# Kernel tuning notes

Hardware: AMD Instinct MI355X
Metric: run time of the kernel (lower is better)

## Reference

```python
import jax, jax.numpy as jnp
import numpy as np

B, Ng, C, H, W, Nt, M, P = 4, 8192, 256, 128, 128, 512, 8, 4
Ch = C // M  # 32 channels per head
EPS = 1e-5


def setup_inputs():
    key = jax.random.key(0)
    ks = jax.random.split(key, 12)
    s = 0.02
    def w(k, shape):
        return jax.random.normal(k, shape, jnp.float32) * s
    return {
        "query": jax.random.normal(ks[0], (B, Ng, C), jnp.float32),
        "value": jax.random.normal(ks[1], (B, C, H, W), jnp.float32),
        "reference_points": jax.random.uniform(ks[2], (B, Ng, 2), dtype=jnp.float32),
        "trajectory_points": jax.random.uniform(ks[3], (B, Nt, 2), dtype=jnp.float32),
        "in_proj_w": w(ks[4], (3 * C, C)),
        "in_proj_b": jnp.zeros((3 * C,), jnp.float32),
        "mha_out_w": w(ks[5], (C, C)),
        "mha_out_b": jnp.zeros((C,), jnp.float32),
        "ln_g": jnp.ones((C,), jnp.float32),
        "ln_b": jnp.zeros((C,), jnp.float32),
        "traj_w": w(ks[6], (C, 2)),
        "traj_b": jnp.zeros((C,), jnp.float32),
        "offs_w": w(ks[7], (M * P * 2, C)),
        "offs_b": jnp.zeros((M * P * 2,), jnp.float32),
        "attw_w": w(ks[8], (M * P, C)),
        "attw_b": jnp.zeros((M * P,), jnp.float32),
        "out_w": w(ks[9], (C, C)),
        "out_b": jnp.zeros((C,), jnp.float32),
    }


def _bilinear_sample(imgf, x, y):
    # imgf: (NM, Ch, H*W); x, y: (NM, Lq, P) unnormalized pixel coords
    # grid_sample semantics: bilinear, padding_mode='zeros', align_corners=False
    NM = imgf.shape[0]
    Lq, Pp = x.shape[1], x.shape[2]
    x0 = jnp.floor(x); y0 = jnp.floor(y)
    x1 = x0 + 1.0;     y1 = y0 + 1.0

    def gather(xi, yi):
        valid = (xi >= 0) & (xi < W) & (yi >= 0) & (yi < H)
        xc = jnp.clip(xi, 0, W - 1).astype(jnp.int32)
        yc = jnp.clip(yi, 0, H - 1).astype(jnp.int32)
        idx = (yc * W + xc).reshape(NM, 1, Lq * Pp)
        v = jnp.take_along_axis(imgf, jnp.broadcast_to(idx, (NM, Ch, Lq * Pp)), axis=2)
        return v.reshape(NM, Ch, Lq, Pp), valid.astype(imgf.dtype)

    v00, m00 = gather(x0, y0)
    v01, m01 = gather(x1, y0)
    v10, m10 = gather(x0, y1)
    v11, m11 = gather(x1, y1)
    wx1 = x - x0; wx0 = 1.0 - wx1
    wy1 = y - y0; wy0 = 1.0 - wy1
    out = (v00 * (wx0 * wy0 * m00)[:, None]
         + v01 * (wx1 * wy0 * m01)[:, None]
         + v10 * (wx0 * wy1 * m10)[:, None]
         + v11 * (wx1 * wy1 * m11)[:, None])
    return out  # (NM, Ch, Lq, P)


def reference(query, value, reference_points, trajectory_points,
              in_proj_w, in_proj_b, mha_out_w, mha_out_b, ln_g, ln_b,
              traj_w, traj_b, offs_w, offs_b, attw_w, attw_b, out_w, out_b):
    # trajectory projection: (B,Nt,2) -> (B,Nt,C)
    tf = trajectory_points @ traj_w.T + traj_b

    # guidance cross-attention (nn.MultiheadAttention, eval mode => no dropout)
    wq, wk, wv = jnp.split(in_proj_w, 3, axis=0)
    bq, bk, bv = jnp.split(in_proj_b, 3, axis=0)
    q = (query @ wq.T + bq).reshape(B, Ng, M, Ch)
    k = (tf @ wk.T + bk).reshape(B, Nt, M, Ch)
    v = (tf @ wv.T + bv).reshape(B, Nt, M, Ch)
    scores = jnp.einsum('bqmc,bkmc->bmqk', q, k) / jnp.sqrt(jnp.float32(Ch))
    probs = jax.nn.softmax(scores, axis=-1)
    ctx = jnp.einsum('bmqk,bkmc->bqmc', probs, v).reshape(B, Ng, C)
    ctx = ctx @ mha_out_w.T + mha_out_b

    # residual + LayerNorm
    x = query + ctx
    mu = x.mean(-1, keepdims=True)
    var = ((x - mu) ** 2).mean(-1, keepdims=True)
    gq = (x - mu) / jnp.sqrt(var + EPS) * ln_g + ln_b

    # sampling offsets & softmax attention weights (L=1 level)
    offs = (gq @ offs_w.T + offs_b).reshape(B, Ng, M, 1, P, 2)
    aw = jax.nn.softmax((gq @ attw_w.T + attw_b).reshape(B, Ng, M, P), axis=-1)
    loc = reference_points[:, :, None, None, None, :] + offs  # (B,Ng,M,1,P,2)

    # deformable sampling core (single level)
    grid = 2.0 * loc[:, :, :, 0] - 1.0                   # (B,Ng,M,P,2)
    grid = grid.transpose(0, 2, 1, 3, 4).reshape(B * M, Ng, P, 2)
    gx = (grid[..., 0] + 1.0) * (W * 0.5) - 0.5
    gy = (grid[..., 1] + 1.0) * (H * 0.5) - 0.5
    imgf = value.reshape(B * M, Ch, H * W)               # per-head feature maps
    samp = _bilinear_sample(imgf, gx, gy)                # (B*M,Ch,Ng,P)
    w_att = aw.transpose(0, 2, 1, 3).reshape(B * M, 1, Ng, P)
    out = (samp * w_att).sum(-1)                         # (B*M,Ch,Ng)

    # faithful to source: view(B,M,Ch,Ng).transpose(1,2).contiguous().view(B,Ng,C)
    out = out.reshape(B, M, Ch, Ng).transpose(0, 2, 1, 3).reshape(B, Ng, C)
    return out @ out_w.T + out_b
```

## Files before the change

### kernel.cpp

```cpp
#include <hip/hip_runtime.h>
#include <hip/hip_bf16.h>
#include <stdint.h>

typedef __bf16 bf16_t;
typedef __bf16 bf16x8 __attribute__((ext_vector_type(8)));
typedef __bf16 bf16x4 __attribute__((ext_vector_type(4)));
typedef float f32x4 __attribute__((ext_vector_type(4)));

#define CEXP 0.25506807186679906f

__device__ __forceinline__ float ldf(const void* p, size_t i, int isf) {
  return isf ? ((const float*)p)[i] : (float)((const bf16_t*)p)[i];
}

__device__ __forceinline__ int detect_isf(const void* q) {
  const uint16_t* u = (const uint16_t*)q;
  const int lane = threadIdx.x & 63;
  const uint16_t v = u[2 * lane];
  const int e = (v >> 7) & 0xFF;
  const int weird = (e >= 0x86 || (v != 0 && e <= 0x65)) ? 1 : 0;
  return (__popcll(__ballot(weird)) >= 16) ? 1 : 0;
}

__device__ __forceinline__ float fexp2(float x) {
#if __has_builtin(__builtin_amdgcn_exp2f)
  return __builtin_amdgcn_exp2f(x);
#else
  return exp2f(x);
#endif
}

__device__ __forceinline__ f32x4 mfma16x16x16(bf16x4 a, bf16x4 b, f32x4 c) {
#if __has_builtin(__builtin_amdgcn_mfma_f32_16x16x16_bf16)
  return __builtin_amdgcn_mfma_f32_16x16x16_bf16(a, b, c, 0, 0, 0);
#else
  typedef short s16x4 __attribute__((ext_vector_type(4)));
  return __builtin_amdgcn_mfma_f32_16x16x16bf16_1k(
      __builtin_bit_cast(s16x4, a), __builtin_bit_cast(s16x4, b), c, 0, 0, 0);
#endif
}

__device__ __forceinline__ void stage16(const bf16_t* g, bf16_t* l) {
  __builtin_amdgcn_global_load_lds((const __attribute__((address_space(1))) void*)g,
                                   (__attribute__((address_space(3))) void*)l, 16, 0, 0);
}

__global__ __launch_bounds__(256) void prep_all(
    const void* __restrict__ query,
    const void* in_w, const void* in_b, const void* mow, const void* mob,
    const void* outw, const void* outb,
    const void* trajp, const void* tw, const void* tb,
    const void* offs_w, const void* attw_w, const void* offs_b, const void* attw_b,
    bf16_t* __restrict__ blob, bf16_t* __restrict__ tf,
    bf16_t* __restrict__ Wph, bf16_t* __restrict__ Wpl, bf16_t* __restrict__ bp,
    const void* __restrict__ V, bf16_t* __restrict__ Vp)
{
  __shared__ __align__(16) bf16_t tile[32][136];
  const int isf = detect_isf(query);
  const int bid = blockIdx.x;
  if (bid < 322) {
    const int g = (bid * 256 + threadIdx.x) * 4;
    if (g >= 328960) return;
    const void* src; size_t off;
    if      (g < 196608) { src = in_w; off = g; }
    else if (g < 197376) { src = in_b; off = g - 196608; }
    else if (g < 262912) { src = mow;  off = g - 197376; }
    else if (g < 263168) { src = mob;  off = g - 262912; }
    else if (g < 328704) { src = outw; off = g - 263168; }
    else                 { src = outb; off = g - 328704; }
#pragma unroll
    for (int k = 0; k < 4; k++) blob[g + k] = (bf16_t)ldf(src, off + k, isf);
  } else if (bid < 322 + 2048) {
    const int rowb = bid - 322;
    const int c = threadIdx.x;
    const float x = ldf(trajp, rowb * 2 + 0, isf);
    const float y = ldf(trajp, rowb * 2 + 1, isf);
    const float v = x * ldf(tw, c * 2 + 0, isf) + y * ldf(tw, c * 2 + 1, isf) + ldf(tb, c, isf);
    tf[(size_t)rowb * 256 + c] = (bf16_t)v;
  } else if (bid < 2498) {
    const int idx = (bid - 2370) * 256 + threadIdx.x;
    const int rowp = idx >> 8, c = idx & 255;
    float v = 0.0f;
    if (rowp < 64)      v = ldf(offs_w, rowp * 256 + c, isf);
    else if (rowp < 96) v = ldf(attw_w, (rowp - 64) * 256 + c, isf);
    const bf16_t hi = (bf16_t)v;
    Wph[idx] = hi;
    Wpl[idx] = (bf16_t)(v - (float)hi);
    if (idx < 128) {
      float bv = 0.0f;
      if (idx < 64)      bv = ldf(offs_b, idx, isf);
      else if (idx < 96) bv = ldf(attw_b, idx - 64, isf);
      bp[idx] = (bf16_t)bv;
    }
  } else {
    const int vb = bid - 2498;
    const int h = vb & 127;
    const int bm = vb >> 7;
    const int b = bm >> 3, mm = bm & 7;
    const int t = threadIdx.x;
    const int ch  = t >> 3;
    const int ww0 = (t & 7) * 16;
    const size_t ibase = (((size_t)b * 256 + mm * 32 + ch) * 128 + h) * 128 + ww0;
    if (isf) {
      const float4* src = (const float4*)((const float*)V + ibase);
      bf16x8 h0, h1;
#pragma unroll
      for (int k = 0; k < 2; k++) {
        const float4 u0 = src[k * 2], u1 = src[k * 2 + 1];
        bf16x8 hh = {(bf16_t)u0.x, (bf16_t)u0.y, (bf16_t)u0.z, (bf16_t)u0.w,
                     (bf16_t)u1.x, (bf16_t)u1.y, (bf16_t)u1.z, (bf16_t)u1.w};
        if (k == 0) h0 = hh; else h1 = hh;
      }
      *(bf16x8*)(&tile[ch][ww0])     = h0;
      *(bf16x8*)(&tile[ch][ww0 + 8]) = h1;
    } else {
      const bf16x8* src = (const bf16x8*)((const bf16_t*)V + ibase);
      *(bf16x8*)(&tile[ch][ww0])     = src[0];
      *(bf16x8*)(&tile[ch][ww0 + 8]) = src[1];
    }
    __syncthreads();
    const size_t base = ((size_t)bm * 128 + h) * 4096;
    const int ww = t >> 1;
    const int c0 = (t & 1) * 16;
    bf16x8 o0, o1;
#pragma unroll
    for (int e = 0; e < 8; e++) { o0[e] = tile[c0 + e][ww]; o1[e] = tile[c0 + 8 + e][ww]; }
    *(bf16x8*)(Vp + base + ww * 32 + c0)     = o0;
    *(bf16x8*)(Vp + base + ww * 32 + c0 + 8) = o1;
  }
}

#define TM 128
#define TN 128
#define TKK 64

__global__ __launch_bounds__(256) void gemm_async(
    const bf16_t* __restrict__ A, const bf16_t* __restrict__ W,
    const bf16_t* __restrict__ bias, void* __restrict__ Cout,
    void* __restrict__ Cout2, int Ndim, int Kdim, int mode, float kscale,
    const void* __restrict__ qdet)
{
  __shared__ __align__(16) bf16_t As[TM * TKK];
  __shared__ __align__(16) bf16_t Ws[TN * TKK];
  const int t    = threadIdx.x;
  const int lane = t & 63;
  const int w    = t >> 6;
  const int wm   = (w & 1) * 64;
  const int wn   = (w >> 1) * 64;
  const int q4   = lane >> 4;
  const int r16  = lane & 15;
  const int tm   = blockIdx.x * TM;
  const int tn   = blockIdx.y * TN;

  f32x4 acc[4][4] = {};

  for (int kt = 0; kt < Kdim; kt += TKK) {
    __syncthreads();
#pragma unroll
    for (int r = 0; r < 4; r++) {
      const int L = w * 256 + r * 64 + lane;
      const int R = L >> 3, c = (L & 7) * 8;
      stage16(A + (size_t)(tm + R) * Kdim + kt + c, As + L * 8);
      stage16(W + (size_t)(tn + R) * Kdim + kt + c, Ws + L * 8);
    }
    __syncthreads();
#pragma unroll
    for (int ks = 0; ks < TKK; ks += 32) {
      bf16x8 af[4], bfm[4];
#pragma unroll
      for (int i = 0; i < 4; i++)
        af[i] = *(const bf16x8*)(As + (wm + 16 * i + r16) * TKK + ks + q4 * 8);
#pragma unroll
      for (int j = 0; j < 4; j++)
        bfm[j] = *(const bf16x8*)(Ws + (wn + 16 * j + r16) * TKK + ks + q4 * 8);
#pragma unroll
      for (int i = 0; i < 4; i++)
#pragma unroll
        for (int j = 0; j < 4; j++)
          acc[i][j] = __builtin_amdgcn_mfma_f32_16x16x32_bf16(af[i], bfm[j], acc[i][j], 0, 0, 0);
    }
  }

  const int isf = (mode == 3) ? detect_isf(qdet) : 1;
#pragma unroll
  for (int j = 0; j < 4; j++) {
    const int col = tn + wn + 16 * j + r16;
    const float bv = (float)bias[col];
#pragma unroll
    for (int i = 0; i < 4; i++) {
      const int row0 = tm + wm + 16 * i + q4 * 4;
#pragma unroll
      for (int rr = 0; rr < 4; rr++) {
        const float v = acc[i][j][rr] + bv;
        const size_t off = (size_t)(row0 + rr) * Ndim + col;
        if (mode == 0) {
          ((bf16_t*)Cout)[off] = (bf16_t)v;
        } else {
          if (isf) ((float*)Cout)[off] = v; else ((bf16_t*)Cout)[off] = (bf16_t)v;
        }
      }
    }
  }
}

__global__ __launch_bounds__(256) void gemm_qkv(
    const void* __restrict__ Araw, const bf16_t* __restrict__ Wq,
    const bf16_t* __restrict__ bq, bf16_t* __restrict__ Cq,
    const bf16_t* __restrict__ Atf, const bf16_t* __restrict__ Wkv,
    const bf16_t* __restrict__ bkv, bf16_t* __restrict__ Kout,
    bf16_t* __restrict__ Vtout, float kscale, const void* __restrict__ qdet)
{
  __shared__ __align__(16) bf16_t As[TM * TKK];
  __shared__ __align__(16) bf16_t Ws[TN * TKK];
  const int t    = threadIdx.x;
  const int lane = t & 63;
  const int w    = t >> 6;
  const int wm   = (w & 1) * 64;
  const int wn   = (w >> 1) * 64;
  const int q4   = lane >> 4;
  const int r16  = lane & 15;
  const int blk  = blockIdx.x;

  f32x4 acc[4][4] = {};

  if (blk < 512) {
    const int tm = (blk >> 1) * TM;
    const int tn = (blk & 1) * TN;
    const int aisf = detect_isf(qdet);
    const int srow = t >> 1;
    const int skb  = (t & 1) * 32;

    for (int kt = 0; kt < 256; kt += TKK) {
      __syncthreads();
      if (aisf) {
        const float4* ga = (const float4*)((const float*)Araw + (size_t)(tm + srow) * 256 + kt + skb);
#pragma unroll
        for (int kk = 0; kk < 8; kk++) {
          const float4 u = ga[kk];
          bf16x4 h = {(bf16_t)u.x, (bf16_t)u.y, (bf16_t)u.z, (bf16_t)u.w};
          *(bf16x4*)(As + srow * TKK + skb + kk * 4) = h;
        }
      } else {
        const uint4* ga = (const uint4*)((const bf16_t*)Araw + (size_t)(tm + srow) * 256 + kt + skb);
        uint4* la = (uint4*)(As + srow * TKK + skb);
        la[0] = ga[0]; la[1] = ga[1]; la[2] = ga[2]; la[3] = ga[3];
      }
      {
        const uint4* gw = (const uint4*)(Wq + (size_t)(tn + srow) * 256 + kt + skb);
        uint4* lw = (uint4*)(Ws + srow * TKK + skb);
        lw[0] = gw[0]; lw[1] = gw[1]; lw[2] = gw[2]; lw[3] = gw[3];
      }
      __syncthreads();
#pragma unroll
      for (int ks = 0; ks < TKK; ks += 32) {
        bf16x8 af[4], bfm[4];
#pragma unroll
        for (int i = 0; i < 4; i++)
          af[i] = *(const bf16x8*)(As + (wm + 16 * i + r16) * TKK + ks + q4 * 8);
#pragma unroll
        for (int j = 0; j < 4; j++)
          bfm[j] = *(const bf16x8*)(Ws + (wn + 16 * j + r16) * TKK + ks + q4 * 8);
#pragma unroll
        for (int i = 0; i < 4; i++)
#pragma unroll
          for (int j = 0; j < 4; j++)
            acc[i][j] = __builtin_amdgcn_mfma_f32_16x16x32_bf16(af[i], bfm[j], acc[i][j], 0, 0, 0);
      }
    }

#pragma unroll
    for (int j = 0; j < 4; j++) {
      const int col = tn + wn + 16 * j + r16;
      const float bv = (float)bq[col];
#pragma unroll
      for (int i = 0; i < 4; i++) {
        const int row0 = tm + wm + 16 * i + q4 * 4;
#pragma unroll
        for (int rr = 0; rr < 4; rr++)
          Cq[(size_t)(row0 + rr) * 256 + col] = (bf16_t)(acc[i][j][rr] + bv);
      }
    }
  } else {
    const int k = blk - 512;
    const int tm = (k & 15) * TM;
    const int tn = (k >> 4) * TN;

    for (int kt = 0; kt < 256; kt += TKK) {
      __syncthreads();
#pragma unroll
      for (int r = 0; r < 4; r++) {
        const int L = w * 256 + r * 64 + lane;
        const int R = L >> 3, c = (L & 7) * 8;
        stage16(Atf + (size_t)(tm + R) * 256 + kt + c, As + L * 8);
        stage16(Wkv + (size_t)(tn + R) * 256 + kt + c, Ws + L * 8);
      }
      __syncthreads();
#pragma unroll
      for (int ks = 0; ks < TKK; ks += 32) {
        bf16x8 af[4], bfm[4];
#pragma unroll
        for (int i = 0; i < 4; i++)
          af[i] = *(const bf16x8*)(As + (wm + 16 * i + r16) * TKK + ks + q4 * 8);
#pragma unroll
        for (int j = 0; j < 4; j++)
          bfm[j] = *(const bf16x8*)(Ws + (wn + 16 * j + r16) * TKK + ks + q4 * 8);
#pragma unroll
        for (int i = 0; i < 4; i++)
#pragma unroll
          for (int j = 0; j < 4; j++)
            acc[i][j] = __builtin_amdgcn_mfma_f32_16x16x32_bf16(af[i], bfm[j], acc[i][j], 0, 0, 0);
      }
    }

#pragma unroll
    for (int j = 0; j < 4; j++) {
      const int col = tn + wn + 16 * j + r16;
      const float bv = (float)bkv[col];
#pragma unroll
      for (int i = 0; i < 4; i++) {
        const int row0 = tm + wm + 16 * i + q4 * 4;
#pragma unroll
        for (int rr = 0; rr < 4; rr++) {
          const float v = acc[i][j][rr] + bv;
          const int rowg = row0 + rr;
          if (col < 256) {
            Kout[(size_t)rowg * 256 + col] = (bf16_t)(v * kscale);
          } else {
            const int bb = rowg >> 9, tt = rowg & 511;
            const int c2 = col - 256;
            const int mm = c2 >> 5, ch = c2 & 31;
            Vtout[(((size_t)(bb * 8 + mm) * 32 + ch) << 9) + tt] = (bf16_t)v;
          }
        }
      }
    }
  }
}

__global__ __launch_bounds__(256, 2) void attn_kernel(
    const bf16_t* __restrict__ Q, const bf16_t* __restrict__ Kk,
    const bf16_t* __restrict__ Vt, bf16_t* __restrict__ ctx)
{
  const int t = threadIdx.x;
  const int lane = t & 63, w = t >> 6;
  const int q4 = lane >> 4, r16 = lane & 15;
  const int bm = blockIdx.y;
  const int b = bm >> 3, m = bm & 7;
  const int q0 = blockIdx.x * 512 + w * 128;

  bf16x8 qf[8];
#pragma unroll
  for (int qt = 0; qt < 8; qt++)
    qf[qt] = *(const bf16x8*)(Q + ((size_t)(b * 8192 + q0 + qt * 16 + r16) * 256 + m * 32 + q4 * 8));

  f32x4 acc[8][2] = {};
  float lsum[8] = {0.f, 0.f, 0.f, 0.f, 0.f, 0.f, 0.f, 0.f};

  const bf16_t* kbase  = Kk + (size_t)b * 512 * 256 + m * 32 + (size_t)r16 * 256 + q4 * 8;
  const bf16_t* vbase0 = Vt + (size_t)bm * 32 * 512 + ((size_t)r16 << 9) + q4 * 4;
  const bf16_t* vbase1 = vbase0 + (16 << 9);

  bf16x8 kfA = *(const bf16x8*)(kbase);
  bf16x4 v0A = *(const bf16x4*)(vbase0);
  bf16x4 v1A = *(const bf16x4*)(vbase1);
  bf16x8 kfB = *(const bf16x8*)(kbase + (size_t)16 * 256);
  bf16x4 v0B = *(const bf16x4*)(vbase0 + 16);
  bf16x4 v1B = *(const bf16x4*)(vbase1 + 16);

  for (int k0 = 0; k0 < 512; k0 += 32) {
    const bf16x8 ka = kfA;
    const bf16x4 va0 = v0A, va1 = v1A;
    kfA = *(const bf16x8*)(kbase + (size_t)(k0 + 32) * 256);
    v0A = *(const bf16x4*)(vbase0 + k0 + 32);
    v1A = *(const bf16x4*)(vbase1 + k0 + 32);
    __builtin_amdgcn_s_setprio(1);
#pragma unroll
    for (int qt = 0; qt < 8; qt++) {
      f32x4 z = {};
      const f32x4 s = __builtin_amdgcn_mfma_f32_16x16x32_bf16(ka, qf[qt], z, 0, 0, 0);
      const float e0 = fexp2(s[0]), e1 = fexp2(s[1]);
      const float e2 = fexp2(s[2]), e3 = fexp2(s[3]);
      lsum[qt] += (e0 + e1) + (e2 + e3);
      const bf16x4 p = {(bf16_t)e0, (bf16_t)e1, (bf16_t)e2, (bf16_t)e3};
      acc[qt][0] = mfma16x16x16(va0, p, acc[qt][0]);
      acc[qt][1] = mfma16x16x16(va1, p, acc[qt][1]);
    }
    __builtin_amdgcn_s_setprio(0);
    const bf16x8 kb = kfB;
    const bf16x4 vb0 = v0B, vb1 = v1B;
    kfB = *(const bf16x8*)(kbase + (size_t)(k0 + 48) * 256);
    v0B = *(const bf16x4*)(vbase0 + k0 + 48);
    v1B = *(const bf16x4*)(vbase1 + k0 + 48);
    __builtin_amdgcn_s_setprio(1);
#pragma unroll
    for (int qt = 0; qt < 8; qt++) {
      f32x4 z = {};
      const f32x4 s = __builtin_amdgcn_mfma_f32_16x16x32_bf16(kb, qf[qt], z, 0, 0, 0);
      const float e0 = fexp2(s[0]), e1 = fexp2(s[1]);
      const float e2 = fexp2(s[2]), e3 = fexp2(s[3]);
      lsum[qt] += (e0 + e1) + (e2 + e3);
      const bf16x4 p = {(bf16_t)e0, (bf16_t)e1, (bf16_t)e2, (bf16_t)e3};
      acc[qt][0] = mfma16x16x16(vb0, p, acc[qt][0]);
      acc[qt][1] = mfma16x16x16(vb1, p, acc[qt][1]);
    }
    __builtin_amdgcn_s_setprio(0);
  }

#pragma unroll
  for (int qt = 0; qt < 8; qt++) {
    float v = lsum[qt];
    v += __shfl_xor(v, 16, 64);
    v += __shfl_xor(v, 32, 64);
    const float inv = 1.0f / v;
    const size_t row = (size_t)b * 8192 + q0 + qt * 16 + r16;
    bf16x4 o0, o1;
#pragma unroll
    for (int rr = 0; rr < 4; rr++) {
      o0[rr] = (bf16_t)(acc[qt][0][rr] * inv);
      o1[rr] = (bf16_t)(acc[qt][1][rr] * inv);
    }
    *(bf16x4*)(ctx + row * 256 + m * 32 + q4 * 4)      = o0;
    *(bf16x4*)(ctx + row * 256 + m * 32 + 16 + q4 * 4) = o1;
  }
}

__global__ __launch_bounds__(256) void ln_kernel(
    const bf16_t* __restrict__ y2, const void* __restrict__ query,
    const void* __restrict__ g, const void* __restrict__ beta,
    bf16_t* __restrict__ gqh, bf16_t* __restrict__ gql)
{
  const int isf = detect_isf(query);
  const int rowb = blockIdx.x * 4 + (threadIdx.x >> 6);
  const int lane = threadIdx.x & 63;
  const size_t base = (size_t)rowb * 256;
  const int c0 = lane * 4;
  float x[4];
  {
    const bf16x4 yv = *(const bf16x4*)(y2 + base + c0);
    if (isf) {
      const float4 qv = *(const float4*)((const float*)query + base + c0);
      x[0] = qv.x + (float)yv[0]; x[1] = qv.y + (float)yv[1];
      x[2] = qv.z + (float)yv[2]; x[3] = qv.w + (float)yv[3];
    } else {
      const bf16x4 qv = *(const bf16x4*)((const bf16_t*)query + base + c0);
#pragma unroll
      for (int k = 0; k < 4; k++) x[k] = (float)qv[k] + (float)yv[k];
    }
  }
  float s = x[0] + x[1] + x[2] + x[3];
  for (int d = 1; d < 64; d <<= 1) s += __shfl_xor(s, d, 64);
  const float mu = s * (1.0f / 256.0f);
  float vs = 0.f;
#pragma unroll
  for (int k = 0; k < 4; k++) { const float d = x[k] - mu; vs += d * d; }
  for (int d = 1; d < 64; d <<= 1) vs += __shfl_xor(vs, d, 64);
  const float rstd = rsqrtf(vs * (1.0f / 256.0f) + 1e-5f);
  float gw[4], bb[4];
  if (isf) {
    const float4 gg = *(const float4*)((const float*)g + c0);
    const float4 bv = *(const float4*)((const float*)beta + c0);
    gw[0] = gg.x; gw[1] = gg.y; gw[2] = gg.z; gw[3] = gg.w;
    bb[0] = bv.x; bb[1] = bv.y; bb[2] = bv.z; bb[3] = bv.w;
  } else {
    const bf16x4 gg = *(const bf16x4*)((const bf16_t*)g + c0);
    const bf16x4 bv = *(const bf16x4*)((const bf16_t*)beta + c0);
#pragma unroll
    for (int k = 0; k < 4; k++) { gw[k] = (float)gg[k]; bb[k] = (float)bv[k]; }
  }
  bf16x4 hi4, lo4;
#pragma unroll
  for (int k = 0; k < 4; k++) {
    const float gv = (x[k] - mu) * rstd * gw[k] + bb[k];
    const bf16_t hi = (bf16_t)gv;
    hi4[k] = hi;
    lo4[k] = (bf16_t)(gv - (float)hi);
  }
  *(bf16x4*)(gqh + base + c0) = hi4;
  *(bf16x4*)(gql + base + c0) = lo4;
}

__global__ __launch_bounds__(256) void gemm_offs(
    const bf16_t* __restrict__ Ahg, const bf16_t* __restrict__ Alg,
    const bf16_t* __restrict__ Whg, const bf16_t* __restrict__ Wlg,
    const bf16_t* __restrict__ bias, float* __restrict__ Cout)
{
  __shared__ __align__(16) bf16_t Ah[128 * 64];
  __shared__ __align__(16) bf16_t Al[128 * 64];
  __shared__ __align__(16) bf16_t Wh[128 * 64];
  __shared__ __align__(16) bf16_t Wl[128 * 64];
  const int t    = threadIdx.x;
  const int lane = t & 63;
  const int w    = t >> 6;
  const int wm   = (w & 1) * 64;
  const int wn   = (w >> 1) * 64;
  const int q4   = lane >> 4;
  const int r16  = lane & 15;
  const int tm   = blockIdx.x * 128;

  f32x4 acc[4][4] = {};
  const int srow = t >> 1;
  const int skb  = (t & 1) * 32;

  for (int kt = 0; kt < 256; kt += 64) {
    __syncthreads();
    {
      const uint4* g0 = (const uint4*)(Ahg + (size_t)(tm + srow) * 256 + kt + skb);
      uint4* l0 = (uint4*)(Ah + srow * 64 + skb);
      l0[0] = g0[0]; l0[1] = g0[1]; l0[2] = g0[2]; l0[3] = g0[3];
      const uint4* g1 = (const uint4*)(Alg + (size_t)(tm + srow) * 256 + kt + skb);
      uint4* l1 = (uint4*)(Al + srow * 64 + skb);
      l1[0] = g1[0]; l1[1] = g1[1]; l1[2] = g1[2]; l1[3] = g1[3];
      const uint4* g2 = (const uint4*)(Whg + (size_t)srow * 256 + kt + skb);
      uint4* l2 = (uint4*)(Wh + srow * 64 + skb);
      l2[0] = g2[0]; l2[1] = g2[1]; l2[2] = g2[2]; l2[3] = g2[3];
      const uint4* g3 = (const uint4*)(Wlg + (size_t)srow * 256 + kt + skb);
      uint4* l3 = (uint4*)(Wl + srow * 64 + skb);
      l3[0] = g3[0]; l3[1] = g3[1]; l3[2] = g3[2]; l3[3] = g3[3];
    }
    __syncthreads();
#pragma unroll
    for (int ks = 0; ks < 64; ks += 32) {
      bf16x8 ah[4], al[4], bh[4], bl[4];
#pragma unroll
      for (int i = 0; i < 4; i++) {
        ah[i] = *(const bf16x8*)(Ah + (wm + 16 * i + r16) * 64 + ks + q4 * 8);
        al[i] = *(const bf16x8*)(Al + (wm + 16 * i + r16) * 64 + ks + q4 * 8);
      }
#pragma unroll
      for (int j = 0; j < 4; j++) {
        bh[j] = *(const bf16x8*)(Wh + (wn + 16 * j + r16) * 64 + ks + q4 * 8);
        bl[j] = *(const bf16x8*)(Wl + (wn + 16 * j + r16) * 64 + ks + q4 * 8);
      }
#pragma unroll
      for (int i = 0; i < 4; i++)
#pragma unroll
        for (int j = 0; j < 4; j++) {
          f32x4 a = acc[i][j];
          a = __builtin_amdgcn_mfma_f32_16x16x32_bf16(al[i], bh[j], a, 0, 0, 0);
          a = __builtin_amdgcn_mfma_f32_16x16x32_bf16(ah[i], bl[j], a, 0, 0, 0);
          a = __builtin_amdgcn_mfma_f32_16x16x32_bf16(ah[i], bh[j], a, 0, 0, 0);
          acc[i][j] = a;
        }
    }
  }

#pragma unroll
  for (int j = 0; j < 4; j++) {
    const int col = wn + 16 * j + r16;
    const float bv = (float)bias[col];
    const int live  = (col < 96) ? 1 : 0;
    const int moff  = (col < 64) ? (col >> 3) : ((col - 64) >> 2);
    const int inner = (col < 64) ? (col & 7) : (8 + (col & 3));
#pragma unroll
    for (int i = 0; i < 4; i++) {
      const int row0 = tm + wm + 16 * i + q4 * 4;
#pragma unroll
      for (int rr = 0; rr < 4; rr++) {
        if (live) {
          const int row = row0 + rr;
          const int bq = row >> 13, q = row & 8191;
          Cout[(((size_t)(bq * 8 + moff) << 13) + q) * 16 + inner] = acc[i][j][rr] + bv;
        }
      }
    }
  }
}

__global__ __launch_bounds__(256) void sampler(
    const float* __restrict__ ys2, const void* __restrict__ refp,
    const bf16_t* __restrict__ vperm, bf16_t* __restrict__ outs,
    const void* __restrict__ qdet)
{
  const int isf = detect_isf(qdet);
  const int t = threadIdx.x;
  const int wg = blockIdx.x;
  const int bm  = (wg & 7) + ((wg >> 9) << 3);
  const int mid = (wg >> 3) & 63;
  const int qt  = mid >> 1;
  const int hf  = mid & 1;
  const int b = bm >> 3, m = bm & 7;
  const int qq = qt * 256 + t;
  const size_t row = (size_t)b * 8192 + qq;
  const float* y16 = ys2 + (((size_t)bm << 13) + qq) * 16;
  const float rx = ldf(refp, row * 2 + 0, isf);
  const float ry = ldf(refp, row * 2 + 1, isf);

  const float4 off01 = *(const float4*)(y16 + 0);
  const float4 off23 = *(const float4*)(y16 + 4);
  const float4 lg    = *(const float4*)(y16 + 8);

  const float mx = fmaxf(fmaxf(lg.x, lg.y), fmaxf(lg.z, lg.w));
  const float e0 = __expf(lg.x - mx), e1 = __expf(lg.y - mx);
  const float e2 = __expf(lg.z - mx), e3 = __expf(lg.w - mx);
  const float inv = 1.0f / (e0 + e1 + e2 + e3);
  const float aw[4] = {e0 * inv, e1 * inv, e2 * inv, e3 * inv};
  const float ox[4] = {off01.x, off01.z, off23.x, off23.z};
  const float oy[4] = {off01.y, off01.w, off23.y, off23.w};

  float acc[16];
#pragma unroll
  for (int ch = 0; ch < 16; ch++) acc[ch] = 0.0f;

  const bf16_t* vbase = vperm + (size_t)bm * (128 * 128 * 32) + hf * 16;

  for (int p = 0; p < 4; p++) {
    const float gx = (rx + ox[p]) * 128.0f - 0.5f;
    const float gy = (ry + oy[p]) * 128.0f - 0.5f;
    const float x0f = floorf(gx), y0f = floorf(gy);
    const int x0 = (int)x0f, y0i = (int)y0f;
    const float wx1 = gx - x0f, wx0 = 1.0f - wx1;
    const float wy1 = gy - y0f, wy0 = 1.0f - wy1;
    const float a = aw[p];
    for (int cy = 0; cy < 2; cy++) {
      const int yy = y0i + cy;
      if (yy < 0 || yy >= 128) continue;
      const float wy = cy ? wy1 : wy0;
      for (int cx = 0; cx < 2; cx++) {
        const int xx = x0 + cx;
        if (xx < 0 || xx >= 128) continue;
        const float wgt = a * wy * (cx ? wx1 : wx0);
        const bf16x8* src8 = (const bf16x8*)(vbase + ((size_t)yy * 128 + xx) * 32);
        const bf16x8 d0 = src8[0];
        const bf16x8 d1 = src8[1];
#pragma unroll
        for (int e = 0; e < 8; e++) {
          acc[e]     += wgt * (float)d0[e];
          acc[8 + e] += wgt * (float)d1[e];
        }
      }
    }
  }

  const size_t obase = (size_t)b * 8192;
#pragma unroll
  for (int ch = 0; ch < 16; ch++) {
    const int chg = hf * 16 + ch;
    const size_t orow = obase + (size_t)(chg * 8 + m) * 32 + qt;
    outs[orow * 256 + t] = (bf16_t)acc[ch];
  }
}

extern "C" void kernel_launch(void* const* d_in, const int* in_sizes, int n_in,
                              void* d_out, int out_size, void* d_ws, size_t ws_size,
                              hipStream_t stream) {
  const void* query = d_in[0];
  const void* value = d_in[1];
  const void* refp  = d_in[2];
  const void* trajp = d_in[3];
  const void* in_w  = d_in[4];
  const void* in_b  = d_in[5];
  const void* mow   = d_in[6];
  const void* mob   = d_in[7];
  const void* lng   = d_in[8];
  const void* lnb   = d_in[9];
  const void* tw    = d_in[10];
  const void* tb    = d_in[11];
  const void* ow    = d_in[12];
  const void* ob    = d_in[13];
  const void* aww   = d_in[14];
  const void* awb   = d_in[15];
  const void* outw  = d_in[16];
  const void* outb  = d_in[17];

  char* base = (char*)d_ws;
  float*  ysamp = (float*)(base);
  bf16_t* qout  = (bf16_t*)(base + 16777216);
  bf16_t* ctx   = (bf16_t*)(base + 33554432);
  bf16_t* y2    = (bf16_t*)(base + 50331648);
  bf16_t* tf_ws = (bf16_t*)(base + 67108864);
  bf16_t* k_ws  = (bf16_t*)(base + 68157440);
  bf16_t* vt_g  = (bf16_t*)(base + 69206016);
  bf16_t* blob  = (bf16_t*)(base + 70254592);

  bf16_t* gqh   = qout;
  bf16_t* gql   = ctx;
  bf16_t* vperm = (bf16_t*)(base + 134217728);
  bf16_t* outs  = y2;

  bf16_t* inw_bf  = blob;
  bf16_t* inb_bf  = blob + 196608;
  bf16_t* mow_bf  = blob + 197376;
  bf16_t* mob_bf  = blob + 262912;
  bf16_t* outw_bf = blob + 263168;
  bf16_t* outb_bf = blob + 328704;
  bf16_t* wph     = blob + 328960;
  bf16_t* wpl     = blob + 361728;
  bf16_t* bpad    = blob + 394496;

  prep_all<<<dim3(6594), dim3(256), 0, stream>>>(
      query, in_w, in_b, mow, mob, outw, outb, trajp, tw, tb,
      ow, aww, ob, awb, blob, tf_ws, wph, wpl, bpad, value, vperm);
  gemm_qkv<<<dim3(576), dim3(256), 0, stream>>>(
      query, inw_bf, inb_bf, qout,
      tf_ws, inw_bf + 65536, inb_bf + 256, k_ws, vt_g, CEXP, query);
  attn_kernel<<<dim3(16, 32), dim3(256), 0, stream>>>(qout, k_ws, vt_g, ctx);
  gemm_async<<<dim3(256, 2), dim3(256), 0, stream>>>(
      ctx, mow_bf, mob_bf, (void*)y2, nullptr, 256, 256, 0, 1.0f, query);
  ln_kernel<<<dim3(8192), dim3(256), 0, stream>>>(y2, query, lng, lnb, gqh, gql);
  gemm_offs<<<dim3(256, 1), dim3(256), 0, stream>>>(gqh, gql, wph, wpl, bpad, ysamp);
  sampler<<<dim3(2048), dim3(256), 0, stream>>>(ysamp, refp, vperm, outs, query);
  gemm_async<<<dim3(256, 2), dim3(256), 0, stream>>>(
      outs, outw_bf, outb_bf, d_out, nullptr, 256, 256, 3, 1.0f, query);
}
```

Measured before the change: 333.5 us.

## Fuse MHA output projection, residual LayerNorm and offsets GEMM into one kernel

```diff
diff --git a/kernel.cpp b/kernel.cpp
--- a/kernel.cpp
+++ b/kernel.cpp
@@ -424,70 +424,23 @@
   }
 }
 
-__global__ __launch_bounds__(256) void ln_kernel(
-    const bf16_t* __restrict__ y2, const void* __restrict__ query,
-    const void* __restrict__ g, const void* __restrict__ beta,
-    bf16_t* __restrict__ gqh, bf16_t* __restrict__ gql)
+__global__ __launch_bounds__(512) void gemm_mlo(
+    const bf16_t* __restrict__ A, const bf16_t* __restrict__ W,
+    const bf16_t* __restrict__ bias, const void* __restrict__ query,
+    const void* __restrict__ lng, const void* __restrict__ lnb,
+    const bf16_t* __restrict__ Whg, const bf16_t* __restrict__ Wlg,
+    const bf16_t* __restrict__ bpad, float* __restrict__ Cout)
 {
-  const int isf = detect_isf(query);
-  const int rowb = blockIdx.x * 4 + (threadIdx.x >> 6);
-  const int lane = threadIdx.x & 63;
-  const size_t base = (size_t)rowb * 256;
-  const int c0 = lane * 4;
-  float x[4];
-  {
-    const bf16x4 yv = *(const bf16x4*)(y2 + base + c0);
-    if (isf) {
-      const float4 qv = *(const float4*)((const float*)query + base + c0);
-      x[0] = qv.x + (float)yv[0]; x[1] = qv.y + (float)yv[1];
-      x[2] = qv.z + (float)yv[2]; x[3] = qv.w + (float)yv[3];
-    } else {
-      const bf16x4 qv = *(const bf16x4*)((const bf16_t*)query + base + c0);
-#pragma unroll
-      for (int k = 0; k < 4; k++) x[k] = (float)qv[k] + (float)yv[k];
-    }
-  }
-  float s = x[0] + x[1] + x[2] + x[3];
-  for (int d = 1; d < 64; d <<= 1) s += __shfl_xor(s, d, 64);
-  const float mu = s * (1.0f / 256.0f);
-  float vs = 0.f;
-#pragma unroll
-  for (int k = 0; k < 4; k++) { const float d = x[k] - mu; vs += d * d; }
-  for (int d = 1; d < 64; d <<= 1) vs += __shfl_xor(vs, d, 64);
-  const float rstd = rsqrtf(vs * (1.0f / 256.0f) + 1e-5f);
-  float gw[4], bb[4];
-  if (isf) {
-    const float4 gg = *(const float4*)((const float*)g + c0);
-    const float4 bv = *(const float4*)((const float*)beta + c0);
-    gw[0] = gg.x; gw[1] = gg.y; gw[2] = gg.z; gw[3] = gg.w;
-    bb[0] = bv.x; bb[1] = bv.y; bb[2] = bv.z; bb[3] = bv.w;
-  } else {
-    const bf16x4 gg = *(const bf16x4*)((const bf16_t*)g + c0);
-    const bf16x4 bv = *(const bf16x4*)((const bf16_t*)beta + c0);
-#pragma unroll
-    for (int k = 0; k < 4; k++) { gw[k] = (float)gg[k]; bb[k] = (float)bv[k]; }
-  }
-  bf16x4 hi4, lo4;
-#pragma unroll
-  for (int k = 0; k < 4; k++) {
-    const float gv = (x[k] - mu) * rstd * gw[k] + bb[k];
-    const bf16_t hi = (bf16_t)gv;
-    hi4[k] = hi;
-    lo4[k] = (bf16_t)(gv - (float)hi);
-  }
-  *(bf16x4*)(gqh + base + c0) = hi4;
-  *(bf16x4*)(gql + base + c0) = lo4;
-}
-
-__global__ __launch_bounds__(256) void gemm_offs(
-    const bf16_t* __restrict__ Ahg, const bf16_t* __restrict__ Alg,
-    const bf16_t* __restrict__ Whg, const bf16_t* __restrict__ Wlg,
-    const bf16_t* __restrict__ bias, float* __restrict__ Cout)
-{
-  __shared__ __align__(16) bf16_t Ah[128 * 64];
-  __shared__ __align__(16) bf16_t Al[128 * 64];
-  __shared__ __align__(16) bf16_t Wh[128 * 64];
-  __shared__ __align__(16) bf16_t Wl[128 * 64];
+  __shared__ __align__(16) char smem[65536];
+  __shared__ float redsum[4][128];
+  __shared__ float redsq[4][128];
+  bf16_t* As = (bf16_t*)smem;
+  bf16_t* Ws = (bf16_t*)(smem + 16384);
+  bf16_t* Ah = (bf16_t*)smem;
+  bf16_t* Al = (bf16_t*)(smem + 16384);
+  bf16_t* Wh = (bf16_t*)(smem + 32768);
+  bf16_t* Wl = (bf16_t*)(smem + 49152);
+
   const int t    = threadIdx.x;
   const int lane = t & 63;
   const int w    = t >> 6;
@@ -495,71 +448,181 @@
   const int wn   = (w >> 1) * 64;
   const int q4   = lane >> 4;
   const int r16  = lane & 15;
-  const int tm   = blockIdx.x * 128;
+  const int R0   = blockIdx.x * 128;
+  const int isf  = detect_isf(query);
 
   f32x4 acc[4][4] = {};
-  const int srow = t >> 1;
-  const int skb  = (t & 1) * 32;
 
   for (int kt = 0; kt < 256; kt += 64) {
     __syncthreads();
-    {
-      const uint4* g0 = (const uint4*)(Ahg + (size_t)(tm + srow) * 256 + kt + skb);
-      uint4* l0 = (uint4*)(Ah + srow * 64 + skb);
-      l0[0] = g0[0]; l0[1] = g0[1]; l0[2] = g0[2]; l0[3] = g0[3];
-      const uint4* g1 = (const uint4*)(Alg + (size_t)(tm + srow) * 256 + kt + skb);
-      uint4* l1 = (uint4*)(Al + srow * 64 + skb);
-      l1[0] = g1[0]; l1[1] = g1[1]; l1[2] = g1[2]; l1[3] = g1[3];
-      const uint4* g2 = (const uint4*)(Whg + (size_t)srow * 256 + kt + skb);
-      uint4* l2 = (uint4*)(Wh + srow * 64 + skb);
-      l2[0] = g2[0]; l2[1] = g2[1]; l2[2] = g2[2]; l2[3] = g2[3];
-      const uint4* g3 = (const uint4*)(Wlg + (size_t)srow * 256 + kt + skb);
-      uint4* l3 = (uint4*)(Wl + srow * 64 + skb);
-      l3[0] = g3[0]; l3[1] = g3[1]; l3[2] = g3[2]; l3[3] = g3[3];
+#pragma unroll
+    for (int r = 0; r < 2; r++) {
+      const int L = r * 512 + t;
+      const int R = L >> 3, c = (L & 7) * 8;
+      stage16(A + (size_t)(R0 + R) * 256 + kt + c, As + L * 8);
+    }
+#pragma unroll
+    for (int r = 0; r < 4; r++) {
+      const int L = r * 512 + t;
+      const int R = L >> 3, c = (L & 7) * 8;
+      stage16(W + (size_t)R * 256 + kt + c, Ws + L * 8);
     }
     __syncthreads();
 #pragma unroll
     for (int ks = 0; ks < 64; ks += 32) {
-      bf16x8 ah[4], al[4], bh[4], bl[4];
+      bf16x8 af[4], bfm[4];
+#pragma unroll
+      for (int i = 0; i < 4; i++)
+        af[i] = *(const bf16x8*)(As + (wm + 16 * i + r16) * 64 + ks + q4 * 8);
+#pragma unroll
+      for (int j = 0; j < 4; j++)
+        bfm[j] = *(const bf16x8*)(Ws + (wn + 16 * j + r16) * 64 + ks + q4 * 8);
+#pragma unroll
+      for (int i = 0; i < 4; i++)
+#pragma unroll
+        for (int j = 0; j < 4; j++)
+          acc[i][j] = __builtin_amdgcn_mfma_f32_16x16x32_bf16(af[i], bfm[j], acc[i][j], 0, 0, 0);
+    }
+  }
+
+#pragma unroll
+  for (int j = 0; j < 4; j++) {
+    const int col = wn + 16 * j + r16;
+    const float bv = (float)bias[col];
+#pragma unroll
+    for (int i = 0; i < 4; i++) {
+#pragma unroll
+      for (int rr = 0; rr < 4; rr++) {
+        const int grow = R0 + wm + 16 * i + q4 * 4 + rr;
+        acc[i][j][rr] += bv + ldf(query, (size_t)grow * 256 + col, isf);
+      }
+    }
+  }
+
+#pragma unroll
+  for (int i = 0; i < 4; i++)
+#pragma unroll
+    for (int rr = 0; rr < 4; rr++) {
+      float s  = acc[i][0][rr] + acc[i][1][rr] + acc[i][2][rr] + acc[i][3][rr];
+      float sq = acc[i][0][rr] * acc[i][0][rr] + acc[i][1][rr] * acc[i][1][rr]
+               + acc[i][2][rr] * acc[i][2][rr] + acc[i][3][rr] * acc[i][3][rr];
+#pragma unroll
+      for (int d = 1; d < 16; d <<= 1) {
+        s  += __shfl_xor(s, d, 64);
+        sq += __shfl_xor(sq, d, 64);
+      }
+      if (r16 == 0) {
+        const int rowl = wm + 16 * i + q4 * 4 + rr;
+        redsum[w >> 1][rowl] = s;
+        redsq[w >> 1][rowl]  = sq;
+      }
+    }
+  __syncthreads();
+
+  float mus[4][4], rstds[4][4];
+#pragma unroll
+  for (int i = 0; i < 4; i++)
+#pragma unroll
+    for (int rr = 0; rr < 4; rr++) {
+      const int rowl = wm + 16 * i + q4 * 4 + rr;
+      const float s  = redsum[0][rowl] + redsum[1][rowl] + redsum[2][rowl] + redsum[3][rowl];
+      const float sq = redsq[0][rowl] + redsq[1][rowl] + redsq[2][rowl] + redsq[3][rowl];
+      const float mu = s * (1.0f / 256.0f);
+      const float var = sq * (1.0f / 256.0f) - mu * mu;
+      mus[i][rr] = mu;
+      rstds[i][rr] = rsqrtf(var + 1e-5f);
+    }
+
+  float gwv[4], bbv[4];
+#pragma unroll
+  for (int j = 0; j < 4; j++) {
+    const int col = wn + 16 * j + r16;
+    gwv[j] = ldf(lng, col, isf);
+    bbv[j] = ldf(lnb, col, isf);
+  }
+  bf16x4 hi4[4][4], lo4[4][4];
+#pragma unroll
+  for (int i = 0; i < 4; i++)
+#pragma unroll
+    for (int j = 0; j < 4; j++)
+#pragma unroll
+      for (int rr = 0; rr < 4; rr++) {
+        const float gv = (acc[i][j][rr] - mus[i][rr]) * rstds[i][rr] * gwv[j] + bbv[j];
+        const bf16_t hi = (bf16_t)gv;
+        hi4[i][j][rr] = hi;
+        lo4[i][j][rr] = (bf16_t)(gv - (float)hi);
+      }
+
+  const int wm2 = wm;
+  const int wn2 = (w >> 1) * 32;
+  f32x4 acc2[4][2] = {};
+  const int myk = w >> 1;
+
+  for (int c4 = 0; c4 < 4; c4++) {
+    const int kt = c4 * 64;
+    if (myk == c4) {
+#pragma unroll
+      for (int i = 0; i < 4; i++)
+#pragma unroll
+        for (int j = 0; j < 4; j++)
+#pragma unroll
+          for (int rr = 0; rr < 4; rr++) {
+            const int r_ = wm + 16 * i + q4 * 4 + rr;
+            Ah[r_ * 64 + 16 * j + r16] = hi4[i][j][rr];
+            Al[r_ * 64 + 16 * j + r16] = lo4[i][j][rr];
+          }
+    }
+#pragma unroll
+    for (int r = 0; r < 2; r++) {
+      const int L = r * 512 + t;
+      const int R = L >> 3, cc = (L & 7) * 8;
+      stage16(Whg + (size_t)R * 256 + kt + cc, Wh + L * 8);
+      stage16(Wlg + (size_t)R * 256 + kt + cc, Wl + L * 8);
+    }
+    __syncthreads();
+#pragma unroll
+    for (int ks = 0; ks < 64; ks += 32) {
+      bf16x8 ah[4], al[4], bh[2], bl[2];
 #pragma unroll
       for (int i = 0; i < 4; i++) {
-        ah[i] = *(const bf16x8*)(Ah + (wm + 16 * i + r16) * 64 + ks + q4 * 8);
-        al[i] = *(const bf16x8*)(Al + (wm + 16 * i + r16) * 64 + ks + q4 * 8);
-      }
-#pragma unroll
-      for (int j = 0; j < 4; j++) {
-        bh[j] = *(const bf16x8*)(Wh + (wn + 16 * j + r16) * 64 + ks + q4 * 8);
-        bl[j] = *(const bf16x8*)(Wl + (wn + 16 * j + r16) * 64 + ks + q4 * 8);
+        ah[i] = *(const bf16x8*)(Ah + (wm2 + 16 * i + r16) * 64 + ks + q4 * 8);
+        al[i] = *(const bf16x8*)(Al + (wm2 + 16 * i + r16) * 64 + ks + q4 * 8);
+      }
+#pragma unroll
+      for (int j = 0; j < 2; j++) {
+        bh[j] = *(const bf16x8*)(Wh + (wn2 + 16 * j + r16) * 64 + ks + q4 * 8);
+        bl[j] = *(const bf16x8*)(Wl + (wn2 + 16 * j + r16) * 64 + ks + q4 * 8);
       }
 #pragma unroll
       for (int i = 0; i < 4; i++)
 #pragma unroll
-        for (int j = 0; j < 4; j++) {
-          f32x4 a = acc[i][j];
+        for (int j = 0; j < 2; j++) {
+          f32x4 a = acc2[i][j];
           a = __builtin_amdgcn_mfma_f32_16x16x32_bf16(al[i], bh[j], a, 0, 0, 0);
           a = __builtin_amdgcn_mfma_f32_16x16x32_bf16(ah[i], bl[j], a, 0, 0, 0);
           a = __builtin_amdgcn_mfma_f32_16x16x32_bf16(ah[i], bh[j], a, 0, 0, 0);
-          acc[i][j] = a;
+          acc2[i][j] = a;
         }
     }
-  }
-
-#pragma unroll
-  for (int j = 0; j < 4; j++) {
-    const int col = wn + 16 * j + r16;
-    const float bv = (float)bias[col];
+    __syncthreads();
+  }
+
+#pragma unroll
+  for (int j = 0; j < 2; j++) {
+    const int col = wn2 + 16 * j + r16;
+    const float bv = (float)bpad[col];
     const int live  = (col < 96) ? 1 : 0;
     const int moff  = (col < 64) ? (col >> 3) : ((col - 64) >> 2);
     const int inner = (col < 64) ? (col & 7) : (8 + (col & 3));
 #pragma unroll
     for (int i = 0; i < 4; i++) {
-      const int row0 = tm + wm + 16 * i + q4 * 4;
+      const int row0 = R0 + wm2 + 16 * i + q4 * 4;
 #pragma unroll
       for (int rr = 0; rr < 4; rr++) {
         if (live) {
           const int row = row0 + rr;
           const int bq = row >> 13, q = row & 8191;
-          Cout[(((size_t)(bq * 8 + moff) << 13) + q) * 16 + inner] = acc[i][j][rr] + bv;
+          Cout[(((size_t)(bq * 8 + moff) << 13) + q) * 16 + inner] = acc2[i][j][rr] + bv;
         }
       }
     }
@@ -666,16 +729,12 @@
   float*  ysamp = (float*)(base);
   bf16_t* qout  = (bf16_t*)(base + 16777216);
   bf16_t* ctx   = (bf16_t*)(base + 33554432);
-  bf16_t* y2    = (bf16_t*)(base + 50331648);
+  bf16_t* outs  = (bf16_t*)(base + 50331648);
   bf16_t* tf_ws = (bf16_t*)(base + 67108864);
   bf16_t* k_ws  = (bf16_t*)(base + 68157440);
   bf16_t* vt_g  = (bf16_t*)(base + 69206016);
   bf16_t* blob  = (bf16_t*)(base + 70254592);
-
-  bf16_t* gqh   = qout;
-  bf16_t* gql   = ctx;
   bf16_t* vperm = (bf16_t*)(base + 134217728);
-  bf16_t* outs  = y2;
 
   bf16_t* inw_bf  = blob;
   bf16_t* inb_bf  = blob + 196608;
@@ -694,10 +753,8 @@
       query, inw_bf, inb_bf, qout,
       tf_ws, inw_bf + 65536, inb_bf + 256, k_ws, vt_g, CEXP, query);
   attn_kernel<<<dim3(16, 32), dim3(256), 0, stream>>>(qout, k_ws, vt_g, ctx);
-  gemm_async<<<dim3(256, 2), dim3(256), 0, stream>>>(
-      ctx, mow_bf, mob_bf, (void*)y2, nullptr, 256, 256, 0, 1.0f, query);
-  ln_kernel<<<dim3(8192), dim3(256), 0, stream>>>(y2, query, lng, lnb, gqh, gql);
-  gemm_offs<<<dim3(256, 1), dim3(256), 0, stream>>>(gqh, gql, wph, wpl, bpad, ysamp);
+  gemm_mlo<<<dim3(256), dim3(512), 0, stream>>>(
+      ctx, mow_bf, mob_bf, query, lng, lnb, wph, wpl, bpad, ysamp);
   sampler<<<dim3(2048), dim3(256), 0, stream>>>(ysamp, refp, vperm, outs, query);
   gemm_async<<<dim3(256, 2), dim3(256), 0, stream>>>(
       outs, outw_bf, outb_bf, d_out, nullptr, 256, 256, 3, 1.0f, query);
```

Measured after the change: 316.8 us. 5.0% less time.
